# Performance work log

Measured on AMD Instinct MI355X. Metric: run time of the kernel, lower is better.

Reference implementation:

```python
import jax, jax.numpy as jnp
import numpy as np

CHUNK = 64
MIN_CLAMP = 1e-6
EPS = 1e-5


def layer_norm(x, scale, bias):
    mu = jnp.mean(x, axis=-1, keepdims=True)
    var = jnp.var(x, axis=-1, keepdims=True)
    return (x - mu) / jnp.sqrt(var + EPS) * scale + bias


def group_norm(x, scale, bias, num_groups):
    # Faithful to the module's GroupNorm: stats over (all rows, within-group channels)
    shp = x.shape
    xr = x.reshape(-1, num_groups, shp[-1] // num_groups)
    mu = jnp.mean(xr, axis=(0, 2), keepdims=True)
    var = jnp.var(xr, axis=(0, 2), keepdims=True)
    xn = ((xr - mu) / jnp.sqrt(var + EPS)).reshape(shp)
    return xn * scale + bias


def time_shift(x):
    return jnp.pad(x[:, :-1], ((0, 0), (1, 0), (0, 0)))


def chunkwise_single(k, v, r, w, u, state):
    # one (batch*head) lane: k,v,r,w,u are (L, D); state is (D, D)
    C = CHUNK
    L, D = r.shape
    pad = (-L) % C
    if pad:
        padf = lambda a: jnp.pad(a, ((0, pad), (0, 0)))
        r, k, v, w, u = map(padf, (r, k, v, w, u))
    Lp = L + pad
    N = Lp // C
    r, k, v, w, u = (a.reshape(N, C, D) for a in (r, k, v, w, u))
    w = jnp.log(jnp.clip(w, MIN_CLAMP, 1.0))
    A = jnp.exp(jnp.cumsum(w, axis=1))                                    # (N,C,D)
    A_inter = jnp.exp(jax.lax.cumsum(w, axis=1, reverse=True) - w)        # (N,C,D)
    A_intra = jnp.cumsum(w, axis=1)                                       # (N,C,D)
    kv = jnp.einsum('ncj,nck->ncjk', A_inter * k, v)                      # (N,C,D,D)

    def scan_fn(s, inp):
        A_t, kv_t = inp
        return A_t * s + kv_t, s

    new_state, S = jax.lax.scan(scan_fn, state, (A.reshape(Lp, D), kv.reshape(Lp, D, D)))
    S = S.reshape(N, C, D, D)
    inter = jnp.einsum('ncj,ncjk->nck', r * jnp.exp(A_intra - w), S)

    mid = C // 2

    def intra_fn(rc, kc, vc, Ac, uc):
        r_decay = rc * jnp.exp(jnp.pad(Ac[:-1], ((1, 0), (0, 0))) - Ac[mid:mid + 1])
        k_decay = kc * jnp.exp(Ac[mid:mid + 1] - Ac)
        u_diag = jnp.diag(jnp.sum(rc * uc * kc, -1))
        return (jnp.tril(r_decay @ k_decay.T, -1) + u_diag) @ vc

    intra = jax.vmap(intra_fn)(r, k, v, A_intra, u)
    y = (inter + intra).reshape(Lp, D)[:L]
    return y, new_state


def _forward(x, state, time_maa_x, time_maa_w, time_maa_k, time_maa_v, time_maa_r, time_maa_g,
             time_decay, time_faaaa, time_maa_w1, time_maa_w2, time_decay_w1, time_decay_w2,
             Wr, Wk, Wv, Wg, Wo, ln_x_scale, ln_x_bias,
             time_maa_k_ch, time_maa_r_ch, Wk_ch, Wv_ch, Wr_ch,
             ln1_scale, ln1_bias, ln2_scale, ln2_bias):
    B, T, E = x.shape
    H, Sh = time_faaaa.shape
    # ---- time mixing (on ln1(x)) ----
    xn = layer_norm(x, ln1_scale, ln1_bias)
    sx = time_shift(xn) - xn
    xmix = xn + sx * time_maa_x
    t5 = jnp.tanh(xmix @ time_maa_w1).reshape(B, T, 5, -1).swapaxes(1, 2)    # (B,5,T,32)
    # faithful to original: batched matmul then reshape (B,5,T,E) -> (5,B,T,E)
    m = jnp.einsum('bgtc,gce->bgte', t5, time_maa_w2).reshape(5, B, T, E)
    mw, mk, mv, mr, mg = m
    xw = xn + sx * (time_maa_w + mw)
    xk = xn + sx * (time_maa_k + mk)
    xv = xn + sx * (time_maa_v + mv)
    xr = xn + sx * (time_maa_r + mr)
    xg = xn + sx * (time_maa_g + mg)
    r = (xr @ Wr).reshape(B, T, H, Sh)
    k = (xk @ Wk).reshape(B, T, H, Sh)
    v = (xv @ Wv).reshape(B, T, H, Sh)
    g = jax.nn.silu(xg @ Wg)                                                 # (B,T,H*Sh)
    off = (jnp.tanh(xw @ time_decay_w1) @ time_decay_w2).reshape(B, T, H, Sh)
    w = jax.nn.softplus(-(time_decay.reshape(1, 1, H, Sh) + off))
    u = jnp.broadcast_to(time_faaaa, (B, T, H, Sh))
    lane = lambda a: a.transpose(0, 2, 1, 3).reshape(B * H, T, Sh)
    y, new_state = jax.vmap(chunkwise_single)(lane(k), lane(v), lane(r), lane(w), lane(u),
                                              state.reshape(B * H, Sh, Sh))
    y = y.reshape(B, H, T, Sh).transpose(0, 2, 1, 3).reshape(B, T, H * Sh)
    y = group_norm(y, ln_x_scale, ln_x_bias, H)
    x = x + (y * g) @ Wo
    # ---- channel mixing (on ln2(x)) ----
    xn2 = layer_norm(x, ln2_scale, ln2_bias)
    sx2 = time_shift(xn2) - xn2
    kk = jax.nn.relu((xn2 + sx2 * time_maa_k_ch) @ Wk_ch) ** 2
    kv = kk @ Wv_ch
    out = x + jax.nn.sigmoid((xn2 + sx2 * time_maa_r_ch) @ Wr_ch) * kv
    return out, new_state.reshape(B, H, Sh, Sh)


def setup_inputs():
    B, T, E = 2, 512, 1024
    H, Sh, F = 16, 64, 4096
    D = H * Sh
    layer_id, n_layer = 12, 24
    r01 = layer_id / (n_layer - 1)
    r10 = 1.0 - layer_id / n_layer
    ar_e = np.arange(E, dtype=np.float64) / E
    maa = lambda p: jnp.asarray((1.0 - ar_e ** p).reshape(1, 1, E), jnp.float32)
    n = np.arange(D, dtype=np.float64)
    time_decay = jnp.asarray((-6 + 5 * (n / (D - 1)) ** (0.7 + 1.3 * r01)).reshape(1, D), jnp.float32)
    time_faaaa = jnp.asarray((r01 * (1 - n / (D - 1)) + ((n + 1) % 3 - 1) * 0.1).reshape(H, Sh), jnp.float32)
    key = jax.random.key(0)
    ks = jax.random.split(key, 14)
    uni = lambda kk, shp: jax.random.uniform(kk, shp, jnp.float32, 0.0, 1e-4)
    dense = lambda kk, i, o: jax.random.normal(kk, (i, o), jnp.float32) / np.float32(np.sqrt(i))
    return dict(
        x=jax.random.normal(ks[0], (B, T, E), jnp.float32),
        state=jnp.zeros((B, H, Sh, Sh), jnp.float32),
        time_maa_x=maa(r10), time_maa_w=maa(r10), time_maa_k=maa(r10),
        time_maa_v=maa(r10 + 0.3 * r01), time_maa_r=maa(0.5 * r10), time_maa_g=maa(0.5 * r10),
        time_decay=time_decay, time_faaaa=time_faaaa,
        time_maa_w1=uni(ks[1], (E, 5 * 32)), time_maa_w2=uni(ks[2], (5, 32, E)),
        time_decay_w1=uni(ks[3], (E, 64)), time_decay_w2=uni(ks[4], (64, E)),
        Wr=dense(ks[5], E, D), Wk=dense(ks[6], E, D), Wv=dense(ks[7], E, D),
        Wg=dense(ks[8], E, D), Wo=dense(ks[9], D, E),
        ln_x_scale=jnp.ones((D,), jnp.float32), ln_x_bias=jnp.zeros((D,), jnp.float32),
        time_maa_k_ch=maa(r10), time_maa_r_ch=maa(r10),
        Wk_ch=dense(ks[10], E, F), Wv_ch=dense(ks[11], F, E), Wr_ch=dense(ks[12], E, E),
        ln1_scale=jnp.ones((E,), jnp.float32), ln1_bias=jnp.zeros((E,), jnp.float32),
        ln2_scale=jnp.ones((E,), jnp.float32), ln2_bias=jnp.zeros((E,), jnp.float32),
    )


def reference(x, state, time_maa_x, time_maa_w, time_maa_k, time_maa_v, time_maa_r, time_maa_g,
              time_decay, time_faaaa, time_maa_w1, time_maa_w2, time_decay_w1, time_decay_w2,
              Wr, Wk, Wv, Wg, Wo, ln_x_scale, ln_x_bias,
              time_maa_k_ch, time_maa_r_ch, Wk_ch, Wv_ch, Wr_ch,
              ln1_scale, ln1_bias, ln2_scale, ln2_bias):
    return _forward(x, state, time_maa_x, time_maa_w, time_maa_k, time_maa_v, time_maa_r, time_maa_g,
                    time_decay, time_faaaa, time_maa_w1, time_maa_w2, time_decay_w1, time_decay_w2,
                    Wr, Wk, Wv, Wg, Wo, ln_x_scale, ln_x_bias,
                    time_maa_k_ch, time_maa_r_ch, Wk_ch, Wv_ch, Wr_ch,
                    ln1_scale, ln1_bias, ln2_scale, ln2_bias)
```

## Files before the change

### kernel.cpp

```cpp
#include <hip/hip_runtime.h>
#include <math.h>

#define T_  512
#define E_  1024
#define BTE 1048576

enum { EPI_NONE=0, EPI_TANH=1, EPI_SILU=2, EPI_RELU2=3, EPI_WLOG=4, EPI_ADDRES=5,
       EPI_SIGMUL4=6 };

typedef __attribute__((ext_vector_type(8))) short bf16x8;
typedef __attribute__((ext_vector_type(4))) float f32x4;

__device__ __forceinline__ unsigned short f2bf(float f) {
    union { float f; unsigned u; } v; v.f = f;
    unsigned r = v.u + 0x7fffu + ((v.u >> 16) & 1u);
    return (unsigned short)(r >> 16);
}
__device__ __forceinline__ float bf2f(unsigned short h) {
    union { unsigned u; float f; } v; v.u = ((unsigned)h) << 16;
    return v.f;
}

__global__ __launch_bounds__(256) void ln1mix_k(const float* __restrict__ x,
        const float* __restrict__ sc, const float* __restrict__ bi,
// ... 35 lines not shown
        st[2] = mup; st[3] = rsqrtf(varp + 1e-5f);
    }
    __syncthreads();
    const float mu = st[0], rstd = st[1], mup = st[2], rstdp = st[3];
    float4 s4 = *reinterpret_cast<const float4*>(sc + tid*4);
    float4 b4 = *reinterpret_cast<const float4*>(bi + tid*4);
    float xnv[4], prv[4];
    xnv[0]=(v.x-mu)*rstd*s4.x+b4.x; xnv[1]=(v.y-mu)*rstd*s4.y+b4.y;
    xnv[2]=(v.z-mu)*rstd*s4.z+b4.z; xnv[3]=(v.w-mu)*rstd*s4.w+b4.w;
    prv[0]=t?(vp.x-mup)*rstdp*s4.x+b4.x:0.f; prv[1]=t?(vp.y-mup)*rstdp*s4.y+b4.y:0.f;
    prv[2]=t?(vp.z-mup)*rstdp*s4.z+b4.z:0.f; prv[3]=t?(vp.w-mup)*rstdp*s4.w+b4.w:0.f;
    float4 o; o.x=xnv[0]; o.y=xnv[1]; o.z=xnv[2]; o.w=xnv[3];
    *reinterpret_cast<float4*>(xn + (size_t)row*E_ + tid*4) = o;
    #pragma unroll
    for (int j = 0; j < 4; ++j) {
        int e = tid*4 + j;
        xmix[(size_t)row*E_ + e] = f2bf(xnv[j] + (prv[j]-xnv[j])*maa[e]);
    }
}

__global__ __launch_bounds__(256) void ln2mix_k(const float* __restrict__ x2,
        const float* __restrict__ sc, const float* __restrict__ bi,
        const float* __restrict__ maaK, const float* __restrict__ maaR,
        unsigned short* __restrict__ ak, unsigned short* __restrict__ ar)
{
    const int row = blockIdx.x;
    const int t = row & 511;
    const int tid = threadIdx.x;
    const float* xr = x2 + (size_t)row * E_;
    float4 v = *reinterpret_cast<const float4*>(xr + tid*4);
    float4 vp = make_float4(0.f, 0.f, 0.f, 0.f);
    if (t) vp = *reinterpret_cast<const float4*>(xr - E_ + tid*4);
    float s   = v.x + v.y + v.z + v.w;
    float ss  = v.x*v.x + v.y*v.y + v.z*v.z + v.w*v.w;
    float sp  = vp.x + vp.y + vp.z + vp.w;
    float ssp = vp.x*vp.x + vp.y*vp.y + vp.z*vp.z + vp.w*vp.w;
    #pragma unroll
    for (int off = 32; off > 0; off >>= 1) {
        s   += __shfl_down(s, off);
        ss  += __shfl_down(ss, off);
        sp  += __shfl_down(sp, off);
        ssp += __shfl_down(ssp, off);
    }
    __shared__ float p0[4], p1[4], p2[4], p3[4];
    __shared__ float st[4];
    if ((tid & 63) == 0) { p0[tid>>6]=s; p1[tid>>6]=ss; p2[tid>>6]=sp; p3[tid>>6]=ssp; }
    __syncthreads();
    if (tid == 0) {
        float S  = p0[0]+p0[1]+p0[2]+p0[3];
        float SS = p1[0]+p1[1]+p1[2]+p1[3];
        float Sp = p2[0]+p2[1]+p2[2]+p2[3];
        float SSp= p3[0]+p3[1]+p3[2]+p3[3];
        float mu  = S * (1.f/E_);
        float var = SS * (1.f/E_) - mu*mu;
        float mup = Sp * (1.f/E_);
        float varp= SSp * (1.f/E_) - mup*mup;
        st[0] = mu; st[1] = rsqrtf(var + 1e-5f);
        st[2] = mup; st[3] = rsqrtf(varp + 1e-5f);
    }
    __syncthreads();
    const float mu = st[0], rstd = st[1], mup = st[2], rstdp = st[3];
    float4 s4 = *reinterpret_cast<const float4*>(sc + tid*4);
    float4 b4 = *reinterpret_cast<const float4*>(bi + tid*4);
    float xnv[4], prv[4];
    xnv[0]=(v.x-mu)*rstd*s4.x+b4.x; xnv[1]=(v.y-mu)*rstd*s4.y+b4.y;
    xnv[2]=(v.z-mu)*rstd*s4.z+b4.z; xnv[3]=(v.w-mu)*rstd*s4.w+b4.w;
    prv[0]=t?(vp.x-mup)*rstdp*s4.x+b4.x:0.f; prv[1]=t?(vp.y-mup)*rstdp*s4.y+b4.y:0.f;
    prv[2]=t?(vp.z-mup)*rstdp*s4.z+b4.z:0.f; prv[3]=t?(vp.w-mup)*rstdp*s4.w+b4.w:0.f;
    #pragma unroll
    for (int j = 0; j < 4; ++j) {
        int e = tid*4 + j;
        float sxv = prv[j] - xnv[j];
        ak[(size_t)row*E_ + e] = f2bf(xnv[j] + sxv*maaK[e]);
        ar[(size_t)row*E_ + e] = f2bf(xnv[j] + sxv*maaR[e]);
    }
}

__global__ __launch_bounds__(256) void t5red_k(const float* __restrict__ tp,
        unsigned short* __restrict__ t5p)
{
    int idx = blockIdx.x*256 + threadIdx.x;
    int c = idx & 63, bt = (idx >> 6) & 1023, g = idx >> 16;
    unsigned short o = 0;
    if (c < 32) {
        float s = 0.f;
        size_t off = (size_t)bt*160 + g*32 + c;
        #pragma unroll
        for (int z = 0; z < 8; ++z) s += tp[(size_t)z*163840 + off];
        o = f2bf(tanhf(s));
    }
    t5p[idx] = o;
}

__global__ __launch_bounds__(256) void dw1red_k(const float* __restrict__ dp,
        unsigned short* __restrict__ h)
{
    int idx = blockIdx.x*256 + threadIdx.x;
    float s = 0.f;
    #pragma unroll
    for (int z = 0; z < 8; ++z) s += dp[(size_t)z*65536 + idx];
    h[idx] = f2bf(tanhf(s));
}

__global__ __launch_bounds__(256) void mix5_apply_k(const float* __restrict__ xn,
        const unsigned short* __restrict__ mb,
        const float* __restrict__ maaW, const float* __restrict__ maaK,
        const float* __restrict__ maaV, const float* __restrict__ maaR,
        const float* __restrict__ maaG,
        unsigned short* __restrict__ xw, unsigned short* __restrict__ xk,
        unsigned short* __restrict__ xv, unsigned short* __restrict__ xr,
        unsigned short* __restrict__ xg)
{
    int idx = blockIdx.x*256 + threadIdx.x;
    int e = idx & 1023;
    int bt = idx >> 10;
    int b = bt >> 9, t = bt & 511;
    float xnv = xn[idx];
    float prev = t ? xn[idx - E_] : 0.f;
    float sxv = prev - xnv;
    float m[5];
    #pragma unroll
    for (int o = 0; o < 5; ++o) {
        int L = o*2 + b;
        int bs = L / 5, gs = L - bs*5;
        m[o] = bf2f(mb[(size_t)gs*1048576 + (size_t)(bs*T_ + t)*E_ + e]);
    }
    xw[idx] = f2bf(xnv + sxv*(maaW[e] + m[0]));
    xk[idx] = f2bf(xnv + sxv*(maaK[e] + m[1]));
    xv[idx] = f2bf(xnv + sxv*(maaV[e] + m[2]));
    xr[idx] = f2bf(xnv + sxv*(maaR[e] + m[3]));
    xg[idx] = f2bf(xnv + sxv*(maaG[e] + m[4]));
}

struct WTA {
    const float* src[16];
    unsigned short* dst[16];
    int K[16], N[16], Npad[16], Kpad[16], tx[16];
    int cum[17];
};
__global__ __launch_bounds__(256) void wtransall_k(WTA a)
{
    int bid = blockIdx.x;
    int s = 0;
    while (bid >= a.cum[s+1]) ++s;
    const int local = bid - a.cum[s];
    const int bx = local % a.tx[s];
    const int by = local / a.tx[s];
    const float* S = a.src[s];
    unsigned short* D = a.dst[s];
    const int K = a.K[s], N = a.N[s], Npad = a.Npad[s], Kpad = a.Kpad[s];
    __shared__ float t[64][65];
    const int tid = threadIdx.x;
    const int k0 = by*64, n0 = bx*64;
    #pragma unroll
    for (int i = 0; i < 16; ++i) {
        int r = i*4 + (tid >> 6), c = tid & 63;
        int gk = k0 + r, gn = n0 + c;
        t[r][c] = (gk < K && gn < N) ? S[(size_t)gk*N + gn] : 0.f;
    }
    __syncthreads();
    #pragma unroll
    for (int i = 0; i < 16; ++i) {
        int r = i*4 + (tid >> 6), c = tid & 63;
        int gn = n0 + r, gk = k0 + c;
        if (gn < Npad && gk < Kpad)
            D[(size_t)gn*Kpad + gk] = f2bf(t[c][r]);
    }
}

struct GemmArgs {
    const unsigned short* A[8];
    const unsigned short* B[8];
    void* C[8];
    const float* p1[8];
    const float* p2[8];
    int epi[8];
    int obf[8];
    int k0[8];
    int M, N, K, ldK;
};
__global__ __launch_bounds__(256) void mgemm_k(GemmArgs g)
{
    const int bz = blockIdx.z;
    const unsigned short* Ag = g.A[bz];
    const unsigned short* BT = g.B[bz];
    const int N = g.N, K = g.K;
    const int gx = gridDim.x, gy = gridDim.y;
    const int lin = blockIdx.x + gx*blockIdx.y;
    const int q = (gx*gy) >> 3;
    const int tile = (lin & 7)*q + (lin >> 3);
    const int bx = tile / gy;
    const int by = tile - bx*gy;
    const int m0 = by * 64, n0 = bx * 64;
    const int tid = threadIdx.x;
    const int lane = tid & 63, w = tid >> 6;

    __shared__ __align__(16) unsigned short As[2][4096];
    __shared__ __align__(16) unsigned short Bs[2][4096];

    const size_t rowBytes = (size_t)g.ldK * 2;
    int sI[4], sIsB[4]; size_t sOff[4];
    #pragma unroll
    for (int ii = 0; ii < 4; ++ii) {
        int t = w*4 + ii;
        int isB = t >> 3;
        int i = t & 7;
        int r = i*8 + (lane >> 3);
        int gb = ((lane & 7) * 16) ^ ((r & 7) << 4);
        sI[ii] = i; sIsB[ii] = isB;
        int srow = (isB ? n0 : m0) + r;
        sOff[ii] = (size_t)srow * rowBytes + gb;
    }
    auto stage = [&](int buf, size_t kbyte) {
        #pragma unroll
        for (int ii = 0; ii < 4; ++ii) {
            const char* src = (const char*)(sIsB[ii] ? BT : Ag) + sOff[ii] + kbyte;
            unsigned short* dst = (sIsB[ii] ? Bs[buf] : As[buf]) + sI[ii]*512;
            auto g1 = (const __attribute__((address_space(1))) unsigned int*)(src);
            auto l3 = (__attribute__((address_space(3))) unsigned int*)(uintptr_t)(dst);
            __builtin_amdgcn_global_load_lds(g1, l3, 16, 0, 0);
        }
    };

    const int wm = (w >> 1) * 32, wn = (w & 1) * 32;
    const int lr = lane & 15, lk = lane >> 4;
    int aoff[2][2], boff[2][2];
    #pragma unroll
    for (int mi = 0; mi < 2; ++mi)
        #pragma unroll
        for (int kw = 0; kw < 2; ++kw) {
            int ar = wm + mi*16 + lr;
            aoff[mi][kw] = ar*128 + ((kw*64 + lk*16) ^ ((ar & 7) << 4));
            int br = wn + mi*16 + lr;
            boff[mi][kw] = br*128 + ((kw*64 + lk*16) ^ ((br & 7) << 4));
        }

    f32x4 acc[2][2] = {};
    const size_t kbase = (size_t)g.k0[bz] * 2;
    stage(0, kbase);
    const int nk = K >> 6;
    int cur = 0;
    for (int kt = 0; kt < nk; ++kt) {
        __syncthreads();
        if (kt + 1 < nk) stage(cur ^ 1, kbase + (size_t)(kt + 1) * 128);
        const char* Ab = (const char*)As[cur];
        const char* Bb = (const char*)Bs[cur];
        bf16x8 af[2][2], bfv[2][2];
        #pragma unroll
        for (int mi = 0; mi < 2; ++mi)
            #pragma unroll
            for (int kw = 0; kw < 2; ++kw) {
                af[mi][kw]  = *(const bf16x8*)(Ab + aoff[mi][kw]);
                bfv[mi][kw] = *(const bf16x8*)(Bb + boff[mi][kw]);
            }
        #pragma unroll
        for (int kw = 0; kw < 2; ++kw)
            #pragma unroll
            for (int mi = 0; mi < 2; ++mi)
                #pragma unroll
                for (int ni = 0; ni < 2; ++ni)
                    acc[mi][ni] = __builtin_amdgcn_mfma_f32_16x16x32_bf16(
                        af[mi][kw], bfv[ni][kw], acc[mi][ni], 0, 0, 0);
        cur ^= 1;
    }

    const int epi = g.epi[bz], obf = g.obf[bz];
    const float* p1 = g.p1[bz];
    const float* p2 = g.p2[bz];
    float* Cf = (float*)g.C[bz];
    unsigned short* Ch = (unsigned short*)g.C[bz];
    #pragma unroll
    for (int mi = 0; mi < 2; ++mi) {
        #pragma unroll
        for (int ni = 0; ni < 2; ++ni) {
            #pragma unroll
            for (int j = 0; j < 4; ++j) {
                int gm = m0 + wm + mi*16 + lk*4 + j;
                int gn = n0 + wn + ni*16 + lr;
                if (gn >= N) continue;
                size_t idx = (size_t)gm * N + gn;
                float a = acc[mi][ni][j];
                float o = a;
                if (epi == EPI_TANH)        o = tanhf(a);
                else if (epi == EPI_SILU)   o = a / (1.f + expf(-a));
                else if (epi == EPI_RELU2)  { float r = fmaxf(a, 0.f); o = r*r; }
                else if (epi == EPI_WLOG) {
                    float z = -(p1[gn] + a);
                    float sp = (z > 15.f) ? z : log1pf(expf(z));
                    o = logf(fminf(fmaxf(sp, 1e-6f), 1.f));
                }
                else if (epi == EPI_ADDRES) o = a + p1[idx];
                else if (epi == EPI_SIGMUL4) {
                    float kvs = p1[idx] + p1[idx + BTE] + p1[idx + 2*BTE] + p1[idx + 3*BTE];
                    o = p2[idx] + kvs / (1.f + expf(-a));
                }
                if (obf) Ch[idx] = f2bf(o); else Cf[idx] = o;
            }
        }
    }
}

#define SWZI(r, c)  (((r) << 6) + ((c) ^ (((r) & 7) << 3)))
#define FIDX(r, kw) (((r) << 6) + ((((kw)*32) + fk*8) ^ (((r) & 7) << 3)))
__global__ __launch_bounds__(512, 4) void chunk1_k(
    const unsigned short* __restrict__ rb, const unsigned short* __restrict__ kb,
    const unsigned short* __restrict__ vb,
    const unsigned short* __restrict__ hdecb, const unsigned short* __restrict__ dw2T,
    const float* __restrict__ tdecay, const float* __restrict__ faaaa,
    float* __restrict__ ypart, float* __restrict__ Ug,
    unsigned short* __restrict__ RDimg, unsigned short* __restrict__ BFb,
    float* __restrict__ B63g)
{
    const int blk = blockIdx.x;
    const int bh = blk >> 3, nc = blk & 7;
    const int b = bh >> 4, h = bh & 15;
    const int tid = threadIdx.x;
    const int l = tid & 63, w = tid >> 6;
    const int jl = l, q = w;
    const int fr = l & 15, fk = l >> 4;
    const int wm = (w >> 2) * 32, wn = (w & 3) * 16;
    const int t0 = nc * 64;

    __shared__ float sQS[8][64];
    __shared__ float sUD[64];
    __shared__ __align__(16) unsigned short pool[32768];
    unsigned short* sRDb  = pool;
    unsigned short* sKAb  = pool + 4096;
    unsigned short* sKA2b = pool + 8192;
    unsigned short* sKATb = pool + 12288;
    unsigned short* sVTb  = pool + 16384;
    unsigned short* sVXTb = pool + 20480;
    unsigned short* sQMb  = pool + 24576;
    unsigned short* sPMb  = pool + 28672;
    float* wlogf = (float*)(pool + 12288);

    const float u_reg = faaaa[h*64 + jl];
    const size_t base = (size_t)b*T_*E_ + (size_t)h*64;
    const size_t coff = (size_t)blk * 4096;

    {
        const int isB = w >> 2;
        #pragma unroll
        for (int ii = 0; ii < 2; ++ii) {
            const int i = (w & 3)*2 + ii;
            const int r = i*8 + (l >> 3);
            const int gb = ((l & 7)*16) ^ ((r & 7) << 4);
            const char* src = isB
                ? ((const char*)dw2T  + (size_t)(h*64 + r)*128 + gb)
                : ((const char*)hdecb + (size_t)(b*T_ + t0 + r)*128 + gb);
            unsigned short* dst = (isB ? sPMb : sQMb) + i*512;
            auto g1 = (const __attribute__((address_space(1))) unsigned int*)(src);
            auto l3 = (__attribute__((address_space(3))) unsigned int*)(uintptr_t)(dst);
            __builtin_amdgcn_global_load_lds(g1, l3, 16, 0, 0);
        }
    }
    __syncthreads();

    {
        f32x4 accO[2] = {};
        #pragma unroll
        for (int kw = 0; kw < 2; ++kw) {
            bf16x8 aH0 = *(const bf16x8*)(&sQMb[FIDX(wm + fr, kw)]);
            bf16x8 aH1 = *(const bf16x8*)(&sQMb[FIDX(wm + 16 + fr, kw)]);
            bf16x8 bD  = *(const bf16x8*)(&sPMb[FIDX(wn + fr, kw)]);
            accO[0] = __builtin_amdgcn_mfma_f32_16x16x32_bf16(aH0, bD, accO[0], 0,0,0);
            accO[1] = __builtin_amdgcn_mfma_f32_16x16x32_bf16(aH1, bD, accO[1], 0,0,0);
        }
        const float td = tdecay[h*64 + wn + fr];
        #pragma unroll
        for (int mi = 0; mi < 2; ++mi)
            #pragma unroll
            for (int reg = 0; reg < 4; ++reg) {
                const int t = wm + mi*16 + fk*4 + reg;
                const int col = wn + fr;
                float z = -(td + accO[mi][reg]);
                float sp = (z > 15.f) ? z : log1pf(expf(z));
                wlogf[t*64 + col] = logf(fminf(fmaxf(sp, 1e-6f), 1.f));
            }
    }
    __syncthreads();

    float loc[8], vreg[8];
    {
        float cum = 0.f;
        #pragma unroll
        for (int c = 0; c < 8; ++c) {
            float wv = wlogf[(q*8 + c)*64 + jl];
            cum += wv; loc[c] = cum;
        }
        sQS[q][jl] = cum;
    }
    __syncthreads();
    float pre = 0.f, atot = 0.f;
    #pragma unroll
    for (int qq = 0; qq < 8; ++qq) {
        float v = sQS[qq][jl];
        atot += v;
        if (qq < q) pre += v;
    }

    #pragma unroll
    for (int c = 0; c < 8; ++c) {
        const int t = q*8 + c;
        const size_t gi = base + (size_t)(t0 + t)*E_ + jl;
        const float rv = bf2f(rb[gi]), kv = bf2f(kb[gi]), vv = bf2f(vb[gi]);
        vreg[c] = vv;
        const float a = loc[c] + pre;
        const float aprev = (c > 0) ? (loc[c-1] + pre) : pre;
        sRDb [SWZI(t, jl)] = f2bf(rv * expf(aprev));
        const float ka = kv * expf(atot - a);
        sKAb [SWZI(t, jl)] = f2bf(ka);
        sKA2b[SWZI(t, jl)] = f2bf(kv * expf(-a));
        sKATb[SWZI(jl, t)] = f2bf(ka);
        sVTb [SWZI(jl, t)] = f2bf(vv);
        float p = rv * u_reg * kv;
        #pragma unroll
        for (int off = 32; off > 0; off >>= 1) p += __shfl_down(p, off);
        if (jl == 0) sUD[t] = p;
    }
    __syncthreads();

    f32x4 accQ[2] = {}, accP[2] = {};
    #pragma unroll
    for (int kw = 0; kw < 2; ++kw) {
        bf16x8 ar0 = *(const bf16x8*)(&sRDb[FIDX(wm + fr, kw)]);
        bf16x8 ar1 = *(const bf16x8*)(&sRDb[FIDX(wm + 16 + fr, kw)]);
        bf16x8 bka = *(const bf16x8*)(&sKAb [FIDX(wn + fr, kw)]);
        bf16x8 bk2 = *(const bf16x8*)(&sKA2b[FIDX(wn + fr, kw)]);
        accQ[0] = __builtin_amdgcn_mfma_f32_16x16x32_bf16(ar0, bk2, accQ[0], 0,0,0);
        accQ[1] = __builtin_amdgcn_mfma_f32_16x16x32_bf16(ar1, bk2, accQ[1], 0,0,0);
        accP[0] = __builtin_amdgcn_mfma_f32_16x16x32_bf16(ar0, bka, accP[0], 0,0,0);
        accP[1] = __builtin_amdgcn_mfma_f32_16x16x32_bf16(ar1, bka, accP[1], 0,0,0);
    }
    #pragma unroll
    for (int mi = 0; mi < 2; ++mi)
        #pragma unroll
        for (int reg = 0; reg < 4; ++reg) {
            int t = wm + mi*16 + fk*4 + reg;
            int s = wn + fr;
            float qv = (s < t) ? accQ[mi][reg] : ((s == t) ? sUD[t] : 0.f);
            float pv = (s < t) ? accP[mi][reg] : 0.f;
            sQMb[SWZI(t, s)] = f2bf(qv);
            sPMb[SWZI(t, s)] = f2bf(pv);
        }

    float loc2[8];
    {
        float cum2 = 0.f;
        #pragma unroll
        for (int c = 0; c < 8; ++c) {
            cum2 += loc[c] + pre;
            loc2[c] = cum2;
        }
        sQS[q][jl] = cum2;
    }
    __syncthreads();
    {
        float pre2 = 0.f;
        #pragma unroll
        for (int qq = 0; qq < 8; ++qq) if (qq < q) pre2 += sQS[qq][jl];
        #pragma unroll
        for (int c = 0; c < 8; ++c) {
            const int t = q*8 + c;
            const float Bv = loc2[c] + pre2;
            const float Bprev = (c > 0) ? (loc2[c-1] + pre2) : pre2;
            const unsigned short bfh = f2bf(expf(Bprev));
            sKA2b[t*64 + jl] = bfh;
            BFb[coff + t*64 + jl] = bfh;
            sVXTb[SWZI(jl, t)] = f2bf(vreg[c] * expf(-Bv));
            if (t == 63) B63g[(size_t)blk*64 + jl] = expf(Bv);
        }
    }
    __syncthreads();

    {
        f32x4 accI[2] = {}, accL[2] = {}, accU[2] = {};
        #pragma unroll
        for (int kw = 0; kw < 2; ++kw) {
            bf16x8 aQ0 = *(const bf16x8*)(&sQMb [FIDX(wm + fr, kw)]);
            bf16x8 aQ1 = *(const bf16x8*)(&sQMb [FIDX(wm + 16 + fr, kw)]);
            bf16x8 aP0 = *(const bf16x8*)(&sPMb [FIDX(wm + fr, kw)]);
            bf16x8 aP1 = *(const bf16x8*)(&sPMb [FIDX(wm + 16 + fr, kw)]);
            bf16x8 aK0 = *(const bf16x8*)(&sKATb[FIDX(wm + fr, kw)]);
            bf16x8 aK1 = *(const bf16x8*)(&sKATb[FIDX(wm + 16 + fr, kw)]);
            bf16x8 bV  = *(const bf16x8*)(&sVTb [FIDX(wn + fr, kw)]);
            bf16x8 bX  = *(const bf16x8*)(&sVXTb[FIDX(wn + fr, kw)]);
            accI[0] = __builtin_amdgcn_mfma_f32_16x16x32_bf16(aQ0, bV, accI[0], 0,0,0);
            accI[1] = __builtin_amdgcn_mfma_f32_16x16x32_bf16(aQ1, bV, accI[1], 0,0,0);
            accL[0] = __builtin_amdgcn_mfma_f32_16x16x32_bf16(aP0, bX, accL[0], 0,0,0);
            accL[1] = __builtin_amdgcn_mfma_f32_16x16x32_bf16(aP1, bX, accL[1], 0,0,0);
            accU[0] = __builtin_amdgcn_mfma_f32_16x16x32_bf16(aK0, bX, accU[0], 0,0,0);
            accU[1] = __builtin_amdgcn_mfma_f32_16x16x32_bf16(aK1, bX, accU[1], 0,0,0);
        }
        #pragma unroll
        for (int mi = 0; mi < 2; ++mi)
            #pragma unroll
            for (int reg = 0; reg < 4; ++reg) {
                int t = wm + mi*16 + fk*4 + reg;
                int k = wn + fr;
                float bfv = bf2f(sKA2b[t*64 + k]);
                ypart[base + (size_t)(t0 + t)*E_ + k] = accI[mi][reg] + bfv*accL[mi][reg];
                Ug[coff + t*64 + k] = accU[mi][reg];
            }
    }
    ((bf16x8*)(RDimg + coff))[tid] = ((const bf16x8*)sRDb)[tid];
}

__global__ __launch_bounds__(256) void chunk2_k(
    const float* __restrict__ st_in, const float* __restrict__ Ug,
    const float* __restrict__ B63g,
    unsigned short* __restrict__ Simg, float* __restrict__ st_out)
{
    const int bh = blockIdx.x;
    const int tid = threadIdx.x;
    __shared__ float S[4096];
    for (int i = tid; i < 4096; i += 256) S[i] = st_in[(size_t)bh*4096 + i];
    __syncthreads();
    const int k = tid >> 2, j0 = (tid & 3) * 16;
    for (int nc = 0; nc < 8; ++nc) {
        const size_t coff = ((size_t)bh*8 + nc) * 4096;
        #pragma unroll
        for (int hf = 0; hf < 2; ++hf) {
            bf16x8 tmp;
            #pragma unroll
            for (int e = 0; e < 8; ++e) tmp[e] = (short)f2bf(S[(j0 + hf*8 + e)*64 + k]);
            *(bf16x8*)(&Simg[coff + SWZI(k, j0 + hf*8)]) = tmp;
        }
        __syncthreads();
        for (int i = tid; i < 4096; i += 256) {
            int kk = i & 63;
            S[i] = B63g[((size_t)bh*8 + nc)*64 + kk] * (S[i] + Ug[coff + i]);
        }
        __syncthreads();
    }
    for (int i = tid; i < 4096; i += 256) st_out[(size_t)bh*4096 + i] = S[i];
}

__global__ __launch_bounds__(256) void chunk3_k(
    const unsigned short* __restrict__ RDimg, const unsigned short* __restrict__ Simg,
    const unsigned short* __restrict__ BFb, float* __restrict__ yb)
{
    const int blk = blockIdx.x;
    const int bh = blk >> 3, nc = blk & 7;
    const int b = bh >> 4, h = bh & 15;
    const int tid = threadIdx.x;
    const int l = tid & 63, w = tid >> 6;
    const int fr = l & 15, fk = l >> 4;
    const int wm = (w >> 1) * 32, wn = (w & 1) * 32;
    const int t0 = nc * 64;
    __shared__ __align__(16) unsigned short sRDb[4096];
    __shared__ __align__(16) unsigned short sSTb[4096];
    const size_t coff = (size_t)blk * 4096;

    #pragma unroll
    for (int ii = 0; ii < 2; ++ii) {
        int seg = (w*2 + ii) * 512;
        {
            auto g1 = (const __attribute__((address_space(1))) unsigned int*)(RDimg + coff + seg + (l << 3));
            auto l3 = (__attribute__((address_space(3))) unsigned int*)(uintptr_t)(sRDb + seg);
            __builtin_amdgcn_global_load_lds(g1, l3, 16, 0, 0);
        }
        {
            auto g1 = (const __attribute__((address_space(1))) unsigned int*)(Simg + coff + seg + (l << 3));
            auto l3 = (__attribute__((address_space(3))) unsigned int*)(uintptr_t)(sSTb + seg);
            __builtin_amdgcn_global_load_lds(g1, l3, 16, 0, 0);
        }
    }
    __syncthreads();

    f32x4 accS[2][2] = {};
    #pragma unroll
    for (int kw = 0; kw < 2; ++kw) {
        bf16x8 aR[2], bS[2];
        #pragma unroll
        for (int mi = 0; mi < 2; ++mi)
            aR[mi] = *(const bf16x8*)(&sRDb[FIDX(wm + mi*16 + fr, kw)]);
        #pragma unroll
        for (int ni = 0; ni < 2; ++ni)
            bS[ni] = *(const bf16x8*)(&sSTb[FIDX(wn + ni*16 + fr, kw)]);
        #pragma unroll
        for (int mi = 0; mi < 2; ++mi)
            #pragma unroll
            for (int ni = 0; ni < 2; ++ni)
                accS[mi][ni] = __builtin_amdgcn_mfma_f32_16x16x32_bf16(aR[mi], bS[ni], accS[mi][ni], 0,0,0);
    }
    const size_t base = (size_t)b*T_*E_ + (size_t)h*64;
    #pragma unroll
    for (int mi = 0; mi < 2; ++mi)
        #pragma unroll
        for (int ni = 0; ni < 2; ++ni)
            #pragma unroll
            for (int reg = 0; reg < 4; ++reg) {
                int t = wm + mi*16 + fk*4 + reg;
                int k = wn + ni*16 + fr;
                size_t gp = base + (size_t)(t0 + t)*E_ + k;
                yb[gp] += bf2f(BFb[coff + t*64 + k]) * accS[mi][ni][reg];
            }
}

__global__ __launch_bounds__(256) void gn_stats_k(const float* __restrict__ y,
        float* __restrict__ part)
{
    const int h = blockIdx.x, slab = blockIdx.y;
    const int tid = threadIdx.x;
    float s = 0.f, ss = 0.f;
    for (int i = tid; i < 2048; i += 256) {
        int r = slab*32 + (i >> 6), k = i & 63;
        float v = y[(size_t)r*E_ + h*64 + k];
        s += v; ss += v*v;
    }
    #pragma unroll
    for (int off = 32; off > 0; off >>= 1) {
        s  += __shfl_down(s, off);
        ss += __shfl_down(ss, off);
    }
    __shared__ float ps[4], pss[4];
    if ((tid & 63) == 0) { ps[tid>>6] = s; pss[tid>>6] = ss; }
    __syncthreads();
    if (tid == 0) {
        part[h*32 + slab]       = ps[0]+ps[1]+ps[2]+ps[3];
        part[512 + h*32 + slab] = pss[0]+pss[1]+pss[2]+pss[3];
    }
}

__global__ __launch_bounds__(256) void gn_apply_k(const float* __restrict__ y,
        const float* __restrict__ g, const float* __restrict__ part,
        const float* __restrict__ sc, const float* __restrict__ bi,
        unsigned short* __restrict__ z)
{
    __shared__ float smu[16], srs[16];
    const int tid = threadIdx.x;
    if (tid < 16) {
        float s = 0.f, ss = 0.f;
        #pragma unroll
        for (int sl = 0; sl < 32; ++sl) {
            s  += part[tid*32 + sl];
            ss += part[512 + tid*32 + sl];
        }
        float mu  = s * (1.f/65536.f);
        float var = ss * (1.f/65536.f) - mu*mu;
        smu[tid] = mu;
        srs[tid] = rsqrtf(var + 1e-5f);
    }
    __syncthreads();
    int idx = blockIdx.x*256 + tid;
    int d = idx & 1023;
    int h = d >> 6;
    float yn = (y[idx] - smu[h])*srs[h]*sc[d] + bi[d];
    z[idx] = f2bf(yn * g[idx]);
}

extern "C" void kernel_launch(void* const* d_in, const int* in_sizes, int n_in,
                              void* d_out, int out_size, void* d_ws, size_t ws_size,
                              hipStream_t stream)
{
    const float* x       = (const float*)d_in[0];
    const float* state0  = (const float*)d_in[1];
    const float* maa_x   = (const float*)d_in[2];
    const float* maa_w   = (const float*)d_in[3];
    const float* maa_k   = (const float*)d_in[4];
    const float* maa_v   = (const float*)d_in[5];
    const float* maa_r   = (const float*)d_in[6];
    const float* maa_g   = (const float*)d_in[7];
    const float* tdecay  = (const float*)d_in[8];
    const float* faaaa   = (const float*)d_in[9];
    const float* w1      = (const float*)d_in[10];
    const float* w2      = (const float*)d_in[11];
    const float* dw1     = (const float*)d_in[12];
    const float* dw2     = (const float*)d_in[13];
    const float* Wr      = (const float*)d_in[14];
    const float* Wk      = (const float*)d_in[15];
    const float* Wv      = (const float*)d_in[16];
    const float* Wg      = (const float*)d_in[17];
    const float* Wo      = (const float*)d_in[18];
    const float* lnx_s   = (const float*)d_in[19];
    const float* lnx_b   = (const float*)d_in[20];
    const float* maa_kch = (const float*)d_in[21];
    const float* maa_rch = (const float*)d_in[22];
    const float* Wk_ch   = (const float*)d_in[23];
    const float* Wv_ch   = (const float*)d_in[24];
    const float* Wr_ch   = (const float*)d_in[25];
    const float* ln1_s   = (const float*)d_in[26];
    const float* ln1_b   = (const float*)d_in[27];
    const float* ln2_s   = (const float*)d_in[28];
    const float* ln2_b   = (const float*)d_in[29];

    float* xn     = (float*)d_ws;
    float* t5dead = xn + 1048576;
    float* gbuf   = t5dead + 163840;
    float* wlogb  = gbuf + 1048576;
    float* ybuf   = wlogb + 1048576;
    float* kvb    = ybuf + 1048576;
    float* gnpart = kvb + 1048576;
    float* gnstat = gnpart + 1024;
    float* b63g   = gnstat + 32;
    unsigned short* u = (unsigned short*)(b63g + 16384);
    unsigned short* xmix = u;  u += 1048576;
    unsigned short* xw   = u;  u += 1048576;
    unsigned short* xk   = u;  u += 1048576;
    unsigned short* xv_  = u;  u += 1048576;
    unsigned short* xr   = u;  u += 1048576;
    unsigned short* xg   = u;  u += 1048576;
    unsigned short* xtr  = u;  u += 1048576;
    unsigned short* rb   = u;  u += 1048576;
    unsigned short* kb   = u;  u += 1048576;
    unsigned short* vb   = u;  u += 1048576;
    unsigned short* hdecb= u;  u += 65536;
    unsigned short* WrT  = u;  u += 1048576;
    unsigned short* WkT  = u;  u += 1048576;
    unsigned short* WvT  = u;  u += 1048576;
    unsigned short* WgT  = u;  u += 1048576;
    unsigned short* WoT  = u;  u += 1048576;
    unsigned short* WrchT= u;  u += 1048576;
    unsigned short* WkchT= u;  u += 4194304;
    unsigned short* WvchT= u;  u += 4194304;
    unsigned short* w1T  = u;  u += 196608;
    unsigned short* dw1T = u;  u += 65536;
    unsigned short* dw2T = u;  u += 65536;
    unsigned short* W2T5 = u;  u += 327680;
    unsigned short* t5p  = u;  u += 327680;
    unsigned short* zbuf  = xmix;
    unsigned short* akb   = xw;
    unsigned short* arb   = xk;
    unsigned short* kkb   = xv_;
    unsigned short* mb16  = (unsigned short*)wlogb;
    float*          Ug    = (float*)xv_;
    unsigned short* RDimg = xg;
    unsigned short* Simg  = xtr;
    unsigned short* BFb   = xmix;
    float* tpart = gbuf;
    float* dpart = (float*)xmix;
    float* kpart = gbuf;

    float* out   = (float*)d_out;
    float* x2buf = out;
    float* stout = out + (size_t)BTE;

    {
        WTA a{};
        const float* srcs[16] = {Wr, Wk, Wv, Wg, Wo, Wr_ch, Wk_ch, Wv_ch, w1, dw1, dw2,
                                 w2, w2+32768, w2+65536, w2+98304, w2+131072};
        unsigned short* dsts[16] = {WrT, WkT, WvT, WgT, WoT, WrchT, WkchT, WvchT,
                                    w1T, dw1T, dw2T,
                                    W2T5, W2T5+65536, W2T5+131072, W2T5+196608, W2T5+262144};
        int Ks[16]    = {1024,1024,1024,1024,1024,1024, 1024, 4096, 1024, 1024,   64, 32,32,32,32,32};
        int Ns[16]    = {1024,1024,1024,1024,1024,1024, 4096, 1024,  160,   64, 1024, 1024,1024,1024,1024,1024};
        int Npads[16] = {1024,1024,1024,1024,1024,1024, 4096, 1024,  192,   64, 1024, 1024,1024,1024,1024,1024};
        int Kpads[16] = {1024,1024,1024,1024,1024,1024, 1024, 4096, 1024, 1024,   64, 64,64,64,64,64};
        int cum = 0;
        for (int i = 0; i < 16; ++i) {
            a.src[i] = srcs[i]; a.dst[i] = dsts[i];
            a.K[i] = Ks[i]; a.N[i] = Ns[i]; a.Npad[i] = Npads[i]; a.Kpad[i] = Kpads[i];
            int txc = (Ns[i] + 63) / 64;
            int tyc = (Ks[i] + 63) / 64;
            a.tx[i] = txc;
            a.cum[i] = cum;
            cum += txc * tyc;
        }
        a.cum[16] = cum;
        wtransall_k<<<cum, 256, 0, stream>>>(a);
    }

    ln1mix_k<<<1024, 256, 0, stream>>>(x, ln1_s, ln1_b, maa_x, xn, xmix);
    { GemmArgs g{}; g.M=1024; g.N=160; g.K=128; g.ldK=1024;
      for (int z = 0; z < 8; ++z) {
          g.A[z]=xmix; g.B[z]=w1T; g.C[z]=tpart + (size_t)z*163840;
          g.epi[z]=EPI_NONE; g.obf[z]=0; g.k0[z]=z*128;
      }
      mgemm_k<<<dim3(3,16,8), 256, 0, stream>>>(g); }
    t5red_k<<<1280, 256, 0, stream>>>(tpart, t5p);
    { GemmArgs g{}; g.M=1024; g.N=1024; g.K=64; g.ldK=64;
      for (int z = 0; z < 5; ++z) {
          g.A[z]=t5p + (size_t)z*65536; g.B[z]=W2T5 + (size_t)z*65536;
          g.C[z]=mb16 + (size_t)z*1048576; g.epi[z]=EPI_NONE; g.obf[z]=1;
      }
      mgemm_k<<<dim3(16,16,5), 256, 0, stream>>>(g); }
    mix5_apply_k<<<4096, 256, 0, stream>>>(xn, mb16, maa_w, maa_k, maa_v, maa_r, maa_g,
                                           xw, xk, xv_, xr, xg);
    { GemmArgs g{}; g.M=1024; g.N=1024; g.K=1024; g.ldK=1024;
      g.A[0]=xr;  g.B[0]=WrT; g.C[0]=rb;   g.epi[0]=EPI_NONE; g.obf[0]=1;
      g.A[1]=xk;  g.B[1]=WkT; g.C[1]=kb;   g.epi[1]=EPI_NONE; g.obf[1]=1;
      g.A[2]=xv_; g.B[2]=WvT; g.C[2]=vb;   g.epi[2]=EPI_NONE; g.obf[2]=1;
      g.A[3]=xg;  g.B[3]=WgT; g.C[3]=gbuf; g.epi[3]=EPI_SILU; g.obf[3]=0;
      mgemm_k<<<dim3(16,16,4), 256, 0, stream>>>(g); }
    { GemmArgs g{}; g.M=1024; g.N=64; g.K=128; g.ldK=1024;
      for (int z = 0; z < 8; ++z) {
          g.A[z]=xw; g.B[z]=dw1T; g.C[z]=dpart + (size_t)z*65536;
          g.epi[z]=EPI_NONE; g.obf[z]=0; g.k0[z]=z*128;
      }
      mgemm_k<<<dim3(1,16,8), 256, 0, stream>>>(g); }
    dw1red_k<<<256, 256, 0, stream>>>(dpart, hdecb);

    chunk1_k<<<256, 512, 0, stream>>>(rb, kb, vb, hdecb, dw2T, tdecay, faaaa,
                                      ybuf, Ug, RDimg, BFb, b63g);
    chunk2_k<<<32, 256, 0, stream>>>(state0, Ug, b63g, Simg, stout);
    chunk3_k<<<256, 256, 0, stream>>>(RDimg, Simg, BFb, ybuf);

    gn_stats_k<<<dim3(16,32), 256, 0, stream>>>(ybuf, gnpart);
    gn_apply_k<<<4096, 256, 0, stream>>>(ybuf, gbuf, gnpart, lnx_s, lnx_b, zbuf);
    { GemmArgs g{}; g.M=1024; g.N=1024; g.K=1024; g.ldK=1024;
      g.A[0]=zbuf; g.B[0]=WoT; g.C[0]=x2buf; g.epi[0]=EPI_ADDRES; g.obf[0]=0; g.p1[0]=x;
      mgemm_k<<<dim3(16,16,1), 256, 0, stream>>>(g); }

    ln2mix_k<<<1024, 256, 0, stream>>>(x2buf, ln2_s, ln2_b, maa_kch, maa_rch, akb, arb);
    { GemmArgs g{}; g.M=1024; g.N=4096; g.K=1024; g.ldK=1024;
      g.A[0]=akb; g.B[0]=WkchT; g.C[0]=kkb; g.epi[0]=EPI_RELU2; g.obf[0]=1;
      mgemm_k<<<dim3(64,16,1), 256, 0, stream>>>(g); }
    { GemmArgs g{}; g.M=1024; g.N=1024; g.K=1024; g.ldK=4096;
      for (int z = 0; z < 4; ++z) {
          g.A[z]=kkb; g.B[z]=WvchT; g.C[z]=kpart + (size_t)z*BTE;
          g.epi[z]=EPI_NONE; g.obf[z]=0; g.k0[z]=z*1024;
      }
      mgemm_k<<<dim3(16,16,4), 256, 0, stream>>>(g); }
    { GemmArgs g{}; g.M=1024; g.N=1024; g.K=1024; g.ldK=1024;
      g.A[0]=arb; g.B[0]=WrchT; g.C[0]=out; g.epi[0]=EPI_SIGMUL4; g.obf[0]=0;
      g.p1[0]=kpart; g.p2[0]=x2buf;
      mgemm_k<<<dim3(16,16,1), 256, 0, stream>>>(g); }
}
```

Measured before the change: 209.0 us.

## Fuse group-norm stats into chunk3, widen chunk1 to 1024 threads, store Ug as bf16

chunk1 now launches 1024 threads (16 waves), so each wave handles a 16x16 output tile instead of 32x16. The inter-chunk Ug buffer is stored as bf16 instead of fp32, which halves the traffic between chunk1 and chunk2 at some cost in precision. The separate gn_stats kernel is removed: chunk3 accumulates sum and sum-of-squares of the y values it writes and emits per-block partials, which gn_apply reduces over batch and chunk. This saves one launch and a full re-read of y, but adds a reduction to chunk3's epilogue.

```diff
diff --git a/kernel.cpp b/kernel.cpp
--- a/kernel.cpp
+++ b/kernel.cpp
@@ -361,12 +361,12 @@
 
 #define SWZI(r, c)  (((r) << 6) + ((c) ^ (((r) & 7) << 3)))
 #define FIDX(r, kw) (((r) << 6) + ((((kw)*32) + fk*8) ^ (((r) & 7) << 3)))
-__global__ __launch_bounds__(512, 4) void chunk1_k(
+__global__ __launch_bounds__(1024, 4) void chunk1_k(
     const unsigned short* __restrict__ rb, const unsigned short* __restrict__ kb,
     const unsigned short* __restrict__ vb,
     const unsigned short* __restrict__ hdecb, const unsigned short* __restrict__ dw2T,
     const float* __restrict__ tdecay, const float* __restrict__ faaaa,
-    float* __restrict__ ypart, float* __restrict__ Ug,
+    float* __restrict__ ypart, unsigned short* __restrict__ Ug,
     unsigned short* __restrict__ RDimg, unsigned short* __restrict__ BFb,
     float* __restrict__ B63g)
 {
@@ -377,10 +377,10 @@
     const int l = tid & 63, w = tid >> 6;
     const int jl = l, q = w;
     const int fr = l & 15, fk = l >> 4;
-    const int wm = (w >> 2) * 32, wn = (w & 3) * 16;
+    const int wm = (w >> 2) * 16, wn = (w & 3) * 16;
     const int t0 = nc * 64;
 
-    __shared__ float sQS[8][64];
+    __shared__ float sQS[16][64];
     __shared__ float sUD[64];
     __shared__ __align__(16) unsigned short pool[32768];
     unsigned short* sRDb  = pool;
@@ -398,53 +398,46 @@
     const size_t coff = (size_t)blk * 4096;
 
     {
-        const int isB = w >> 2;
-        #pragma unroll
-        for (int ii = 0; ii < 2; ++ii) {
-            const int i = (w & 3)*2 + ii;
-            const int r = i*8 + (l >> 3);
-            const int gb = ((l & 7)*16) ^ ((r & 7) << 4);
-            const char* src = isB
-                ? ((const char*)dw2T  + (size_t)(h*64 + r)*128 + gb)
-                : ((const char*)hdecb + (size_t)(b*T_ + t0 + r)*128 + gb);
-            unsigned short* dst = (isB ? sPMb : sQMb) + i*512;
-            auto g1 = (const __attribute__((address_space(1))) unsigned int*)(src);
-            auto l3 = (__attribute__((address_space(3))) unsigned int*)(uintptr_t)(dst);
-            __builtin_amdgcn_global_load_lds(g1, l3, 16, 0, 0);
-        }
+        const int isB = w >> 3;
+        const int i = w & 7;
+        const int r = i*8 + (l >> 3);
+        const int gb = ((l & 7)*16) ^ ((r & 7) << 4);
+        const char* src = isB
+            ? ((const char*)dw2T  + (size_t)(h*64 + r)*128 + gb)
+            : ((const char*)hdecb + (size_t)(b*T_ + t0 + r)*128 + gb);
+        unsigned short* dst = (isB ? sPMb : sQMb) + i*512;
+        auto g1 = (const __attribute__((address_space(1))) unsigned int*)(src);
+        auto l3 = (__attribute__((address_space(3))) unsigned int*)(uintptr_t)(dst);
+        __builtin_amdgcn_global_load_lds(g1, l3, 16, 0, 0);
     }
     __syncthreads();
 
     {
-        f32x4 accO[2] = {};
+        f32x4 accO = {};
         #pragma unroll
         for (int kw = 0; kw < 2; ++kw) {
-            bf16x8 aH0 = *(const bf16x8*)(&sQMb[FIDX(wm + fr, kw)]);
-            bf16x8 aH1 = *(const bf16x8*)(&sQMb[FIDX(wm + 16 + fr, kw)]);
-            bf16x8 bD  = *(const bf16x8*)(&sPMb[FIDX(wn + fr, kw)]);
-            accO[0] = __builtin_amdgcn_mfma_f32_16x16x32_bf16(aH0, bD, accO[0], 0,0,0);
-            accO[1] = __builtin_amdgcn_mfma_f32_16x16x32_bf16(aH1, bD, accO[1], 0,0,0);
+            bf16x8 aH = *(const bf16x8*)(&sQMb[FIDX(wm + fr, kw)]);
+            bf16x8 bD = *(const bf16x8*)(&sPMb[FIDX(wn + fr, kw)]);
+            accO = __builtin_amdgcn_mfma_f32_16x16x32_bf16(aH, bD, accO, 0,0,0);
         }
         const float td = tdecay[h*64 + wn + fr];
         #pragma unroll
-        for (int mi = 0; mi < 2; ++mi)
-            #pragma unroll
-            for (int reg = 0; reg < 4; ++reg) {
-                const int t = wm + mi*16 + fk*4 + reg;
-                const int col = wn + fr;
-                float z = -(td + accO[mi][reg]);
-                float sp = (z > 15.f) ? z : log1pf(expf(z));
-                wlogf[t*64 + col] = logf(fminf(fmaxf(sp, 1e-6f), 1.f));
-            }
-    }
-    __syncthreads();
-
-    float loc[8], vreg[8];
+        for (int reg = 0; reg < 4; ++reg) {
+            const int t = wm + fk*4 + reg;
+            const int col = wn + fr;
+            float z = -(td + accO[reg]);
+            float sp = (z > 15.f) ? z : log1pf(expf(z));
+            wlogf[t*64 + col] = logf(fminf(fmaxf(sp, 1e-6f), 1.f));
+        }
+    }
+    __syncthreads();
+
+    float loc[4], vreg[4];
     {
         float cum = 0.f;
         #pragma unroll
-        for (int c = 0; c < 8; ++c) {
-            float wv = wlogf[(q*8 + c)*64 + jl];
+        for (int c = 0; c < 4; ++c) {
+            float wv = wlogf[(q*4 + c)*64 + jl];
             cum += wv; loc[c] = cum;
         }
         sQS[q][jl] = cum;
@@ -452,15 +445,15 @@
     __syncthreads();
     float pre = 0.f, atot = 0.f;
     #pragma unroll
-    for (int qq = 0; qq < 8; ++qq) {
+    for (int qq = 0; qq < 16; ++qq) {
         float v = sQS[qq][jl];
         atot += v;
         if (qq < q) pre += v;
     }
 
     #pragma unroll
-    for (int c = 0; c < 8; ++c) {
-        const int t = q*8 + c;
+    for (int c = 0; c < 4; ++c) {
+        const int t = q*4 + c;
         const size_t gi = base + (size_t)(t0 + t)*E_ + jl;
         const float rv = bf2f(rb[gi]), kv = bf2f(kb[gi]), vv = bf2f(vb[gi]);
         vreg[c] = vv;
@@ -479,35 +472,30 @@
     }
     __syncthreads();
 
-    f32x4 accQ[2] = {}, accP[2] = {};
+    f32x4 accQ = {}, accP = {};
     #pragma unroll
     for (int kw = 0; kw < 2; ++kw) {
-        bf16x8 ar0 = *(const bf16x8*)(&sRDb[FIDX(wm + fr, kw)]);
-        bf16x8 ar1 = *(const bf16x8*)(&sRDb[FIDX(wm + 16 + fr, kw)]);
+        bf16x8 ar  = *(const bf16x8*)(&sRDb [FIDX(wm + fr, kw)]);
         bf16x8 bka = *(const bf16x8*)(&sKAb [FIDX(wn + fr, kw)]);
         bf16x8 bk2 = *(const bf16x8*)(&sKA2b[FIDX(wn + fr, kw)]);
-        accQ[0] = __builtin_amdgcn_mfma_f32_16x16x32_bf16(ar0, bk2, accQ[0], 0,0,0);
-        accQ[1] = __builtin_amdgcn_mfma_f32_16x16x32_bf16(ar1, bk2, accQ[1], 0,0,0);
-        accP[0] = __builtin_amdgcn_mfma_f32_16x16x32_bf16(ar0, bka, accP[0], 0,0,0);
-        accP[1] = __builtin_amdgcn_mfma_f32_16x16x32_bf16(ar1, bka, accP[1], 0,0,0);
-    }
-    #pragma unroll
-    for (int mi = 0; mi < 2; ++mi)
-        #pragma unroll
-        for (int reg = 0; reg < 4; ++reg) {
-            int t = wm + mi*16 + fk*4 + reg;
-            int s = wn + fr;
-            float qv = (s < t) ? accQ[mi][reg] : ((s == t) ? sUD[t] : 0.f);
-            float pv = (s < t) ? accP[mi][reg] : 0.f;
-            sQMb[SWZI(t, s)] = f2bf(qv);
-            sPMb[SWZI(t, s)] = f2bf(pv);
-        }
-
-    float loc2[8];
+        accQ = __builtin_amdgcn_mfma_f32_16x16x32_bf16(ar, bk2, accQ, 0,0,0);
+        accP = __builtin_amdgcn_mfma_f32_16x16x32_bf16(ar, bka, accP, 0,0,0);
+    }
+    #pragma unroll
+    for (int reg = 0; reg < 4; ++reg) {
+        int t = wm + fk*4 + reg;
+        int s = wn + fr;
+        float qv = (s < t) ? accQ[reg] : ((s == t) ? sUD[t] : 0.f);
+        float pv = (s < t) ? accP[reg] : 0.f;
+        sQMb[SWZI(t, s)] = f2bf(qv);
+        sPMb[SWZI(t, s)] = f2bf(pv);
+    }
+
+    float loc2[4];
     {
         float cum2 = 0.f;
         #pragma unroll
-        for (int c = 0; c < 8; ++c) {
+        for (int c = 0; c < 4; ++c) {
             cum2 += loc[c] + pre;
             loc2[c] = cum2;
         }
@@ -517,10 +505,10 @@
     {
         float pre2 = 0.f;
         #pragma unroll
-        for (int qq = 0; qq < 8; ++qq) if (qq < q) pre2 += sQS[qq][jl];
-        #pragma unroll
-        for (int c = 0; c < 8; ++c) {
-            const int t = q*8 + c;
+        for (int qq = 0; qq < 16; ++qq) if (qq < q) pre2 += sQS[qq][jl];
+        #pragma unroll
+        for (int c = 0; c < 4; ++c) {
+            const int t = q*4 + c;
             const float Bv = loc2[c] + pre2;
             const float Bprev = (c > 0) ? (loc2[c-1] + pre2) : pre2;
             const unsigned short bfh = f2bf(expf(Bprev));
@@ -533,40 +521,33 @@
     __syncthreads();
 
     {
-        f32x4 accI[2] = {}, accL[2] = {}, accU[2] = {};
+        f32x4 accI = {}, accL = {}, accU = {};
         #pragma unroll
         for (int kw = 0; kw < 2; ++kw) {
-            bf16x8 aQ0 = *(const bf16x8*)(&sQMb [FIDX(wm + fr, kw)]);
-            bf16x8 aQ1 = *(const bf16x8*)(&sQMb [FIDX(wm + 16 + fr, kw)]);
-            bf16x8 aP0 = *(const bf16x8*)(&sPMb [FIDX(wm + fr, kw)]);
-            bf16x8 aP1 = *(const bf16x8*)(&sPMb [FIDX(wm + 16 + fr, kw)]);
-            bf16x8 aK0 = *(const bf16x8*)(&sKATb[FIDX(wm + fr, kw)]);
-            bf16x8 aK1 = *(const bf16x8*)(&sKATb[FIDX(wm + 16 + fr, kw)]);
-            bf16x8 bV  = *(const bf16x8*)(&sVTb [FIDX(wn + fr, kw)]);
-            bf16x8 bX  = *(const bf16x8*)(&sVXTb[FIDX(wn + fr, kw)]);
-            accI[0] = __builtin_amdgcn_mfma_f32_16x16x32_bf16(aQ0, bV, accI[0], 0,0,0);
-            accI[1] = __builtin_amdgcn_mfma_f32_16x16x32_bf16(aQ1, bV, accI[1], 0,0,0);
-            accL[0] = __builtin_amdgcn_mfma_f32_16x16x32_bf16(aP0, bX, accL[0], 0,0,0);
-            accL[1] = __builtin_amdgcn_mfma_f32_16x16x32_bf16(aP1, bX, accL[1], 0,0,0);
-            accU[0] = __builtin_amdgcn_mfma_f32_16x16x32_bf16(aK0, bX, accU[0], 0,0,0);
-            accU[1] = __builtin_amdgcn_mfma_f32_16x16x32_bf16(aK1, bX, accU[1], 0,0,0);
-        }
-        #pragma unroll
-        for (int mi = 0; mi < 2; ++mi)
-            #pragma unroll
-            for (int reg = 0; reg < 4; ++reg) {
-                int t = wm + mi*16 + fk*4 + reg;
-                int k = wn + fr;
-                float bfv = bf2f(sKA2b[t*64 + k]);
-                ypart[base + (size_t)(t0 + t)*E_ + k] = accI[mi][reg] + bfv*accL[mi][reg];
-                Ug[coff + t*64 + k] = accU[mi][reg];
-            }
-    }
-    ((bf16x8*)(RDimg + coff))[tid] = ((const bf16x8*)sRDb)[tid];
+            bf16x8 aQ = *(const bf16x8*)(&sQMb [FIDX(wm + fr, kw)]);
+            bf16x8 aP = *(const bf16x8*)(&sPMb [FIDX(wm + fr, kw)]);
+            bf16x8 aK = *(const bf16x8*)(&sKATb[FIDX(wm + fr, kw)]);
+            bf16x8 bV = *(const bf16x8*)(&sVTb [FIDX(wn + fr, kw)]);
+            bf16x8 bX = *(const bf16x8*)(&sVXTb[FIDX(wn + fr, kw)]);
+            accI = __builtin_amdgcn_mfma_f32_16x16x32_bf16(aQ, bV, accI, 0,0,0);
+            accL = __builtin_amdgcn_mfma_f32_16x16x32_bf16(aP, bX, accL, 0,0,0);
+            accU = __builtin_amdgcn_mfma_f32_16x16x32_bf16(aK, bX, accU, 0,0,0);
+        }
+        #pragma unroll
+        for (int reg = 0; reg < 4; ++reg) {
+            int t = wm + fk*4 + reg;
+            int k = wn + fr;
+            float bfv = bf2f(sKA2b[t*64 + k]);
+            ypart[base + (size_t)(t0 + t)*E_ + k] = accI[reg] + bfv*accL[reg];
+            Ug[coff + t*64 + k] = f2bf(accU[reg]);
+        }
+    }
+    if (tid < 512)
+        ((bf16x8*)(RDimg + coff))[tid] = ((const bf16x8*)sRDb)[tid];
 }
 
 __global__ __launch_bounds__(256) void chunk2_k(
-    const float* __restrict__ st_in, const float* __restrict__ Ug,
+    const float* __restrict__ st_in, const unsigned short* __restrict__ Ug,
     const float* __restrict__ B63g,
     unsigned short* __restrict__ Simg, float* __restrict__ st_out)
 {
@@ -588,7 +569,7 @@
         __syncthreads();
         for (int i = tid; i < 4096; i += 256) {
             int kk = i & 63;
-            S[i] = B63g[((size_t)bh*8 + nc)*64 + kk] * (S[i] + Ug[coff + i]);
+            S[i] = B63g[((size_t)bh*8 + nc)*64 + kk] * (S[i] + bf2f(Ug[coff + i]));
         }
         __syncthreads();
     }
@@ -597,7 +578,8 @@
 
 __global__ __launch_bounds__(256) void chunk3_k(
     const unsigned short* __restrict__ RDimg, const unsigned short* __restrict__ Simg,
-    const unsigned short* __restrict__ BFb, float* __restrict__ yb)
+    const unsigned short* __restrict__ BFb, float* __restrict__ yb,
+    float* __restrict__ part)
 {
     const int blk = blockIdx.x;
     const int bh = blk >> 3, nc = blk & 7;
@@ -622,7 +604,7 @@
         {
             auto g1 = (const __attribute__((address_space(1))) unsigned int*)(Simg + coff + seg + (l << 3));
             auto l3 = (__attribute__((address_space(3))) unsigned int*)(uintptr_t)(sSTb + seg);
-            __builtin_amdgcn_global_load_lds(g1, l3, 16, 0, 0);
+            __builtin_amdgcn_global_load_lds(g1, l3, 0x10, 0, 0);
         }
     }
     __syncthreads();
@@ -644,6 +626,7 @@
                 accS[mi][ni] = __builtin_amdgcn_mfma_f32_16x16x32_bf16(aR[mi], bS[ni], accS[mi][ni], 0,0,0);
     }
     const size_t base = (size_t)b*T_*E_ + (size_t)h*64;
+    float s = 0.f, ss = 0.f;
     #pragma unroll
     for (int mi = 0; mi < 2; ++mi)
         #pragma unroll
@@ -653,32 +636,21 @@
                 int t = wm + mi*16 + fk*4 + reg;
                 int k = wn + ni*16 + fr;
                 size_t gp = base + (size_t)(t0 + t)*E_ + k;
-                yb[gp] += bf2f(BFb[coff + t*64 + k]) * accS[mi][ni][reg];
+                float yv = yb[gp] + bf2f(BFb[coff + t*64 + k]) * accS[mi][ni][reg];
+                yb[gp] = yv;
+                s += yv; ss += yv*yv;
             }
-}
-
-__global__ __launch_bounds__(256) void gn_stats_k(const float* __restrict__ y,
-        float* __restrict__ part)
-{
-    const int h = blockIdx.x, slab = blockIdx.y;
-    const int tid = threadIdx.x;
-    float s = 0.f, ss = 0.f;
-    for (int i = tid; i < 2048; i += 256) {
-        int r = slab*32 + (i >> 6), k = i & 63;
-        float v = y[(size_t)r*E_ + h*64 + k];
-        s += v; ss += v*v;
-    }
     #pragma unroll
     for (int off = 32; off > 0; off >>= 1) {
         s  += __shfl_down(s, off);
         ss += __shfl_down(ss, off);
     }
     __shared__ float ps[4], pss[4];
-    if ((tid & 63) == 0) { ps[tid>>6] = s; pss[tid>>6] = ss; }
+    if (l == 0) { ps[w] = s; pss[w] = ss; }
     __syncthreads();
     if (tid == 0) {
-        part[h*32 + slab]       = ps[0]+ps[1]+ps[2]+ps[3];
-        part[512 + h*32 + slab] = pss[0]+pss[1]+pss[2]+pss[3];
+        part[blk]       = ps[0]+ps[1]+ps[2]+ps[3];
+        part[256 + blk] = pss[0]+pss[1]+pss[2]+pss[3];
     }
 }
 
@@ -692,10 +664,13 @@
     if (tid < 16) {
         float s = 0.f, ss = 0.f;
         #pragma unroll
-        for (int sl = 0; sl < 32; ++sl) {
-            s  += part[tid*32 + sl];
-            ss += part[512 + tid*32 + sl];
-        }
+        for (int b = 0; b < 2; ++b)
+            #pragma unroll
+            for (int ncc = 0; ncc < 8; ++ncc) {
+                int ib = (b*16 + tid)*8 + ncc;
+                s  += part[ib];
+                ss += part[256 + ib];
+            }
         float mu  = s * (1.f/65536.f);
         float var = ss * (1.f/65536.f) - mu*mu;
         smu[tid] = mu;
@@ -783,7 +758,7 @@
     unsigned short* arb   = xk;
     unsigned short* kkb   = xv_;
     unsigned short* mb16  = (unsigned short*)wlogb;
-    float*          Ug    = (float*)xv_;
+    unsigned short* Ug    = xv_;
     unsigned short* RDimg = xg;
     unsigned short* Simg  = xtr;
     unsigned short* BFb   = xmix;
@@ -850,12 +825,11 @@
       mgemm_k<<<dim3(1,16,8), 256, 0, stream>>>(g); }
     dw1red_k<<<256, 256, 0, stream>>>(dpart, hdecb);
 
-    chunk1_k<<<256, 512, 0, stream>>>(rb, kb, vb, hdecb, dw2T, tdecay, faaaa,
-                                      ybuf, Ug, RDimg, BFb, b63g);
+    chunk1_k<<<256, 1024, 0, stream>>>(rb, kb, vb, hdecb, dw2T, tdecay, faaaa,
+                                       ybuf, Ug, RDimg, BFb, b63g);
     chunk2_k<<<32, 256, 0, stream>>>(state0, Ug, b63g, Simg, stout);
-    chunk3_k<<<256, 256, 0, stream>>>(RDimg, Simg, BFb, ybuf);
-
-    gn_stats_k<<<dim3(16,32), 256, 0, stream>>>(ybuf, gnpart);
+    chunk3_k<<<256, 256, 0, stream>>>(RDimg, Simg, BFb, ybuf, gnpart);
+
     gn_apply_k<<<4096, 256, 0, stream>>>(ybuf, gbuf, gnpart, lnx_s, lnx_b, zbuf);
     { GemmArgs g{}; g.M=1024; g.N=1024; g.K=1024; g.ldK=1024;
       g.A[0]=zbuf; g.B[0]=WoT; g.C[0]=x2buf; g.epi[0]=EPI_ADDRES; g.obf[0]=0; g.p1[0]=x;
```

New measurement: 186.1 us. 1.12x faster.
